# Kernel optimization log

Hardware: AMD Instinct MI355X
Metric: run time of the kernel (lower is better)

## Reference

```python
import jax, jax.numpy as jnp
import numpy as np

ALPHA = 8.3  # depth similarity sharpness, F_D = exp(-alpha*|D(p0)-D(pn)|) (depth-aware CNN)
PAD, STRIDE, DIL, KH, KW = 1, 1, 1, 3, 3


def setup_inputs() -> dict:
    key = jax.random.key(0)
    k1, k2, k3, k4 = jax.random.split(key, 4)
    B, C_in, C_out, H, W = 2, 32, 32, 512, 512
    x = jax.random.normal(k1, (B, C_in, H, W), dtype=jnp.float32)
    depth = jax.random.uniform(k2, (B, 1, H, W), dtype=jnp.float32)
    weight = jax.random.normal(k3, (C_out, C_in, KH, KW), dtype=jnp.float32) * 0.05
    bias = jax.random.normal(k4, (C_out,), dtype=jnp.float32) * 0.05
    return {"x": x, "depth": depth, "weight": weight, "bias": bias}


def _depthconv(x, depth, weight, bias):
    B, C, H, W = x.shape
    C_out = weight.shape[0]
    H_out = (H + 2 * PAD - DIL * (KH - 1) - 1) // STRIDE + 1
    W_out = (W + 2 * PAD - DIL * (KW - 1) - 1) // STRIDE + 1
    x_p = jnp.pad(x, ((0, 0), (0, 0), (PAD, PAD), (PAD, PAD)))
    d_p = jnp.pad(depth, ((0, 0), (0, 0), (PAD, PAD), (PAD, PAD)))
    # depth at the receptive-field center of each output pixel, [B,1,H_out,W_out]
    ci, cj = (KH // 2) * DIL, (KW // 2) * DIL
    d_c = d_p[:, :, ci:ci + H_out * STRIDE:STRIDE, cj:cj + W_out * STRIDE:STRIDE]
    out = jnp.broadcast_to(bias[None, :, None, None], (B, C_out, H_out, W_out)).astype(x.dtype)
    for ki in range(KH):
        for kj in range(KW):
            hs, ws = ki * DIL, kj * DIL
            xs = x_p[:, :, hs:hs + H_out * STRIDE:STRIDE, ws:ws + W_out * STRIDE:STRIDE]
            ds = d_p[:, :, hs:hs + H_out * STRIDE:STRIDE, ws:ws + W_out * STRIDE:STRIDE]
            sim = jnp.exp(-ALPHA * jnp.abs(d_c - ds))  # [B,1,H_out,W_out]
            out = out + jnp.einsum('oc,bchw->bohw', weight[:, :, ki, kj], xs * sim)
    return out


def reference(x, depth, weight, bias):
    return _depthconv(x, depth, weight, bias)
```

## Files before the change

kernel.cpp:

```cpp
#include <hip/hip_runtime.h>

typedef _Float16 half8 __attribute__((ext_vector_type(8)));
typedef float floatx4 __attribute__((ext_vector_type(4)));

constexpr int C = 32, H = 512, W = 512, HW = H * W;
constexpr int TBH = 8, TBW = 64;
constexpr int RR  = TBH + 2;
constexpr int PX  = 72;

__device__ __forceinline__ unsigned pack2h(float lo, float hi) {
    unsigned a = (unsigned)__builtin_bit_cast(unsigned short, (_Float16)lo);
    unsigned b = (unsigned)__builtin_bit_cast(unsigned short, (_Float16)hi);
    return a | (b << 16);
}

__global__ __launch_bounds__(256) void pack_w(const float* __restrict__ weight,
                                              uint4* __restrict__ wp) {
    int j = blockIdx.x * 256 + threadIdx.x;
    if (j >= 1152) return;
    int lane = j & 63, half = (j >> 6) & 1, tap = j >> 7;
    int o = half * 16 + (lane & 15), q = lane >> 4;
    uint4 v;
    v.x = pack2h(weight[(o * 32 + q * 8 + 0) * 9 + tap], weight[(o * 32 + q * 8 + 1) * 9 + tap]);
    v.y = pack2h(weight[(o * 32 + q * 8 + 2) * 9 + tap], weight[(o * 32 + q * 8 + 3) * 9 + tap]);
    v.z = pack2h(weight[(o * 32 + q * 8 + 4) * 9 + tap], weight[(o * 32 + q * 8 + 5) * 9 + tap]);
    v.w = pack2h(weight[(o * 32 + q * 8 + 6) * 9 + tap], weight[(o * 32 + q * 8 + 7) * 9 + tap]);
    wp[j] = v;
}

__global__ __launch_bounds__(256, 2) void depthconv_fused(
    const float* __restrict__ x, const float* __restrict__ depth,
    const uint4* __restrict__ wp, const float* __restrict__ bias,
    float* __restrict__ out)
{
    __shared__ __attribute__((aligned(16))) unsigned xsl[RR * PX * 16];
    __shared__ float2 dsim[RR][PX];

    const int bid  = blockIdx.x;
    const int wseg = bid & 7, hseg = (bid >> 3) & 63, b = bid >> 9;
    const int h0 = hseg * TBH, w0 = wseg * TBW;
    const int tid = threadIdx.x;

    for (int u = tid; u < 16 * RR * 18; u += 256) {
        int f4 = u % 18, t = u / 18;
        int r = t % RR, cp = t / RR;
        int h = h0 - 1 + r, wst = w0 - 4 + f4 * 4;
        bool valid = (h >= 0) && (h < H) && (wst >= 0) && (wst < W);
        float4 va = {0.f, 0.f, 0.f, 0.f}, vb = {0.f, 0.f, 0.f, 0.f};
        if (valid) {
            const float* xb = x + ((size_t)(b * C + 2 * cp)) * HW + h * W + wst;
            va = *(const float4*)xb;
            vb = *(const float4*)(xb + HW);
        }
        int swz = (((cp >> 2) ^ (f4 & 3)) << 2) | (cp & 3);
        unsigned* dst = &xsl[(r * PX + f4 * 4) * 16 + swz];
        dst[0]  = pack2h(va.x, vb.x);
        dst[16] = pack2h(va.y, vb.y);
        dst[32] = pack2h(va.z, vb.z);
        dst[48] = pack2h(va.w, vb.w);
    }

    if (tid < RR * 18) {
        int f4 = tid % 18, r = tid / 18;
        int h = h0 - 1 + r, wst = w0 - 4 + f4 * 4;
        bool valid = (h >= 0) && (h < H) && (wst >= 0) && (wst < W);
        float4 dv = {0.f, 0.f, 0.f, 0.f};
        if (valid) dv = *(const float4*)(depth + (size_t)b * HW + h * W + wst);
        float dd[4] = {dv.x, dv.y, dv.z, dv.w};
        #pragma unroll
        for (int j = 0; j < 4; ++j) {
            dsim[r][f4 * 4 + j] = valid
                ? make_float2(__expf(-8.3f * dd[j]), __expf(8.3f * dd[j]))
                : make_float2(0.f, 0.f);
        }
    }

    const int lane = tid & 63, wid = tid >> 6;
    const int nn = lane & 15, q = lane >> 4;

    half8 af[2][9];
    #pragma unroll
    for (int tap = 0; tap < 9; ++tap) {
        af[0][tap] = __builtin_bit_cast(half8, wp[(tap * 2 + 0) * 64 + lane]);
        af[1][tap] = __builtin_bit_cast(half8, wp[(tap * 2 + 1) * 64 + lane]);
    }

    floatx4 acc[TBH][2];
    #pragma unroll
    for (int o = 0; o < TBH; ++o)
        #pragma unroll
        for (int i = 0; i < 4; ++i) {
            acc[o][0][i] = bias[q * 4 + i];
            acc[o][1][i] = bias[16 + q * 4 + i];
        }

    __syncthreads();

    const int pc = wid * 16 + nn;
    float2 dc[TBH];
    #pragma unroll
    for (int o = 0; o < TBH; ++o) dc[o] = dsim[o + 1][pc + 4];

    #pragma unroll
    for (int r = 0; r < RR; ++r) {
        uint4 xraw[3]; float2 dn[3];
        #pragma unroll
        for (int kj = 0; kj < 3; ++kj) {
            int p = pc + 3 + kj;
            xraw[kj] = *(const uint4*)&xsl[(r * PX + p) * 16 + ((q ^ ((p >> 2) & 3)) << 2)];
            dn[kj] = dsim[r][p];
        }
        #pragma unroll
        for (int kj = 0; kj < 3; ++kj) {
            #pragma unroll
            for (int ki = 0; ki < 3; ++ki) {
                int o = r - ki;
                if (o < 0 || o >= TBH) continue;
                int tap = ki * 3 + kj;
                float s = fminf(dn[kj].y * dc[o].x, dn[kj].x * dc[o].y);
                _Float16 hs = (_Float16)s;
                half8 sv = { hs, hs, hs, hs, hs, hs, hs, hs };
                half8 bf = __builtin_bit_cast(half8, xraw[kj]) * sv;
                acc[o][0] = __builtin_amdgcn_mfma_f32_16x16x32_f16(af[0][tap], bf, acc[o][0], 0, 0, 0);
                acc[o][1] = __builtin_amdgcn_mfma_f32_16x16x32_f16(af[1][tap], bf, acc[o][1], 0, 0, 0);
            }
        }
    }

    const int pw = w0 + pc;
    #pragma unroll
    for (int o = 0; o < TBH; ++o) {
        float* op = out + (size_t)b * C * HW + (size_t)(h0 + o) * W + pw;
        #pragma unroll
        for (int i = 0; i < 4; ++i) {
            op[(size_t)(q * 4 + i) * HW]      = acc[o][0][i];
            op[(size_t)(16 + q * 4 + i) * HW] = acc[o][1][i];
        }
    }
}

extern "C" void kernel_launch(void* const* d_in, const int* in_sizes, int n_in,
                              void* d_out, int out_size, void* d_ws, size_t ws_size,
                              hipStream_t stream) {
    const float* x      = (const float*)d_in[0];
    const float* depth  = (const float*)d_in[1];
    const float* weight = (const float*)d_in[2];
    const float* bias   = (const float*)d_in[3];
    float* out          = (float*)d_out;

    uint4* wpk = (uint4*)d_ws;

    hipLaunchKernelGGL(pack_w, dim3(5), dim3(256), 0, stream, weight, wpk);
    hipLaunchKernelGGL(depthconv_fused, dim3(2 * 64 * 8), dim3(256), 0, stream,
                       x, depth, wpk, bias, out);
}
```

Measured before the change: 142.5 us.

## Shrink conv tiles, split output channels across waves, interleave depth into LDS

The block tile shrinks from 8x64 to 4x32 pixels. Each wave now computes half the output channels for 16 pixels, which halves its accumulators and weight registers, and launch bounds rise to four blocks per CU. The LDS layout changes to a padded per-pixel record holding eight channel-pairs plus the depth-similarity pair, replacing the XOR swizzle and the separate depth array. Global loads become scalar strided per-channel reads instead of float4. More halo is reloaded per output pixel, and the narrower loads may coalesce less well.

```diff
diff --git a/kernel.cpp b/kernel.cpp
--- a/kernel.cpp
+++ b/kernel.cpp
@@ -4,9 +4,12 @@
 typedef float floatx4 __attribute__((ext_vector_type(4)));
 
 constexpr int C = 32, H = 512, W = 512, HW = H * W;
-constexpr int TBH = 8, TBW = 64;
+constexpr int TBH = 4;
+constexpr int TBW = 32;
 constexpr int RR  = TBH + 2;
-constexpr int PX  = 72;
+constexpr int PX  = TBW + 8;
+constexpr int PXW = 20;
+constexpr int ROWW = PX * PXW + 8;
 
 __device__ __forceinline__ unsigned pack2h(float lo, float hi) {
     unsigned a = (unsigned)__builtin_bit_cast(unsigned short, (_Float16)lo);
@@ -28,87 +31,77 @@
     wp[j] = v;
 }
 
-__global__ __launch_bounds__(256, 2) void depthconv_fused(
+__global__ __launch_bounds__(256, 4) void depthconv_fused(
     const float* __restrict__ x, const float* __restrict__ depth,
     const uint4* __restrict__ wp, const float* __restrict__ bias,
     float* __restrict__ out)
 {
-    __shared__ __attribute__((aligned(16))) unsigned xsl[RR * PX * 16];
-    __shared__ float2 dsim[RR][PX];
+    __shared__ __attribute__((aligned(16))) unsigned xsl[RR * ROWW];
 
     const int bid  = blockIdx.x;
-    const int wseg = bid & 7, hseg = (bid >> 3) & 63, b = bid >> 9;
+    const int wseg = bid & 15, hseg = (bid >> 4) & 127, b = bid >> 11;
     const int h0 = hseg * TBH, w0 = wseg * TBW;
     const int tid = threadIdx.x;
 
-    for (int u = tid; u < 16 * RR * 18; u += 256) {
-        int f4 = u % 18, t = u / 18;
-        int r = t % RR, cp = t / RR;
-        int h = h0 - 1 + r, wst = w0 - 4 + f4 * 4;
-        bool valid = (h >= 0) && (h < H) && (wst >= 0) && (wst < W);
-        float4 va = {0.f, 0.f, 0.f, 0.f}, vb = {0.f, 0.f, 0.f, 0.f};
-        if (valid) {
-            const float* xb = x + ((size_t)(b * C + 2 * cp)) * HW + h * W + wst;
-            va = *(const float4*)xb;
-            vb = *(const float4*)(xb + HW);
-        }
-        int swz = (((cp >> 2) ^ (f4 & 3)) << 2) | (cp & 3);
-        unsigned* dst = &xsl[(r * PX + f4 * 4) * 16 + swz];
-        dst[0]  = pack2h(va.x, vb.x);
-        dst[16] = pack2h(va.y, vb.y);
-        dst[32] = pack2h(va.z, vb.z);
-        dst[48] = pack2h(va.w, vb.w);
+    const int lane = tid & 63, wid = tid >> 6;
+    const int nn = lane & 15, q = lane >> 4;
+    const int chh = wid >> 1;
+    const int pcl = (wid & 1) * 16 + nn;
+
+    half8 af[9];
+    #pragma unroll
+    for (int tap = 0; tap < 9; ++tap)
+        af[tap] = __builtin_bit_cast(half8, wp[(tap * 2 + chh) * 64 + lane]);
+
+    floatx4 acc[TBH];
+    #pragma unroll
+    for (int i = 0; i < 4; ++i) {
+        float bv = bias[chh * 16 + q * 4 + i];
+        #pragma unroll
+        for (int o = 0; o < TBH; ++o) acc[o][i] = bv;
     }
 
-    if (tid < RR * 18) {
-        int f4 = tid % 18, r = tid / 18;
-        int h = h0 - 1 + r, wst = w0 - 4 + f4 * 4;
-        bool valid = (h >= 0) && (h < H) && (wst >= 0) && (wst < W);
-        float4 dv = {0.f, 0.f, 0.f, 0.f};
-        if (valid) dv = *(const float4*)(depth + (size_t)b * HW + h * W + wst);
-        float dd[4] = {dv.x, dv.y, dv.z, dv.w};
+    for (int u = tid; u < 4 * RR * PX; u += 256) {
+        int px = u % PX, t = u / PX;
+        int r = t % RR, qc = t / RR;
+        int h = h0 - 1 + r, ww = w0 - 4 + px;
+        bool valid = ((unsigned)h < (unsigned)H) && ((unsigned)ww < (unsigned)W);
+        const float* xb = x + ((size_t)(b * C + 8 * qc)) * HW + (size_t)h * W + ww;
+        float v[8];
         #pragma unroll
-        for (int j = 0; j < 4; ++j) {
-            dsim[r][f4 * 4 + j] = valid
-                ? make_float2(__expf(-8.3f * dd[j]), __expf(8.3f * dd[j]))
-                : make_float2(0.f, 0.f);
-        }
+        for (int k = 0; k < 8; ++k)
+            v[k] = valid ? xb[(size_t)k * HW] : 0.f;
+        uint4 o4;
+        o4.x = pack2h(v[0], v[1]); o4.y = pack2h(v[2], v[3]);
+        o4.z = pack2h(v[4], v[5]); o4.w = pack2h(v[6], v[7]);
+        *(uint4*)&xsl[r * ROWW + px * PXW + 4 * qc] = o4;
     }
 
-    const int lane = tid & 63, wid = tid >> 6;
-    const int nn = lane & 15, q = lane >> 4;
-
-    half8 af[2][9];
-    #pragma unroll
-    for (int tap = 0; tap < 9; ++tap) {
-        af[0][tap] = __builtin_bit_cast(half8, wp[(tap * 2 + 0) * 64 + lane]);
-        af[1][tap] = __builtin_bit_cast(half8, wp[(tap * 2 + 1) * 64 + lane]);
+    for (int u = tid; u < RR * PX; u += 256) {
+        int px = u % PX, r = u / PX;
+        int h = h0 - 1 + r, ww = w0 - 4 + px;
+        bool valid = ((unsigned)h < (unsigned)H) && ((unsigned)ww < (unsigned)W);
+        float d = valid ? depth[(size_t)b * HW + (size_t)h * W + ww] : 0.f;
+        float2 e = valid ? make_float2(__expf(-8.3f * d), __expf(8.3f * d))
+                         : make_float2(0.f, 0.f);
+        *(float2*)&xsl[r * ROWW + px * PXW + 16] = e;
     }
-
-    floatx4 acc[TBH][2];
-    #pragma unroll
-    for (int o = 0; o < TBH; ++o)
-        #pragma unroll
-        for (int i = 0; i < 4; ++i) {
-            acc[o][0][i] = bias[q * 4 + i];
-            acc[o][1][i] = bias[16 + q * 4 + i];
-        }
 
     __syncthreads();
 
-    const int pc = wid * 16 + nn;
     float2 dc[TBH];
     #pragma unroll
-    for (int o = 0; o < TBH; ++o) dc[o] = dsim[o + 1][pc + 4];
+    for (int o = 0; o < TBH; ++o)
+        dc[o] = *(const float2*)&xsl[(o + 1) * ROWW + (pcl + 4) * PXW + 16];
 
     #pragma unroll
     for (int r = 0; r < RR; ++r) {
         uint4 xraw[3]; float2 dn[3];
         #pragma unroll
         for (int kj = 0; kj < 3; ++kj) {
-            int p = pc + 3 + kj;
-            xraw[kj] = *(const uint4*)&xsl[(r * PX + p) * 16 + ((q ^ ((p >> 2) & 3)) << 2)];
-            dn[kj] = dsim[r][p];
+            int p = pcl + 3 + kj;
+            xraw[kj] = *(const uint4*)&xsl[r * ROWW + p * PXW + 4 * q];
+            dn[kj]   = *(const float2*)&xsl[r * ROWW + p * PXW + 16];
         }
         #pragma unroll
         for (int kj = 0; kj < 3; ++kj) {
@@ -121,21 +114,18 @@
                 _Float16 hs = (_Float16)s;
                 half8 sv = { hs, hs, hs, hs, hs, hs, hs, hs };
                 half8 bf = __builtin_bit_cast(half8, xraw[kj]) * sv;
-                acc[o][0] = __builtin_amdgcn_mfma_f32_16x16x32_f16(af[0][tap], bf, acc[o][0], 0, 0, 0);
-                acc[o][1] = __builtin_amdgcn_mfma_f32_16x16x32_f16(af[1][tap], bf, acc[o][1], 0, 0, 0);
+                acc[o] = __builtin_amdgcn_mfma_f32_16x16x32_f16(af[tap], bf, acc[o], 0, 0, 0);
             }
         }
     }
 
-    const int pw = w0 + pc;
+    const int pw = w0 + pcl;
     #pragma unroll
     for (int o = 0; o < TBH; ++o) {
         float* op = out + (size_t)b * C * HW + (size_t)(h0 + o) * W + pw;
         #pragma unroll
-        for (int i = 0; i < 4; ++i) {
-            op[(size_t)(q * 4 + i) * HW]      = acc[o][0][i];
-            op[(size_t)(16 + q * 4 + i) * HW] = acc[o][1][i];
-        }
+        for (int i = 0; i < 4; ++i)
+            op[(size_t)(chh * 16 + q * 4 + i) * HW] = acc[o][i];
     }
 }
 
@@ -151,6 +141,6 @@
     uint4* wpk = (uint4*)d_ws;
 
     hipLaunchKernelGGL(pack_w, dim3(5), dim3(256), 0, stream, weight, wpk);
-    hipLaunchKernelGGL(depthconv_fused, dim3(2 * 64 * 8), dim3(256), 0, stream,
+    hipLaunchKernelGGL(depthconv_fused, dim3(2 * 128 * 16), dim3(256), 0, stream,
                        x, depth, wpk, bias, out);
 }
```

Measured after the change: 180.1 us. +26.4%, slower.
